# Performance work log

Measured on AMD Instinct MI355X. Metric: run time of the kernel, lower is better.

The kernel has to match this reference:

```python
import jax, jax.numpy as jnp
import numpy as np
from jax import lax

B, H, W = 1, 128, 128
KS = 3
N = KS * KS  # 9 deformable sampling points
BN_EPS = 1e-5


def conv2d(x, w, padding=0, stride=1):
    return lax.conv_general_dilated(x, w, (stride, stride),
                                    [(padding, padding), (padding, padding)],
                                    dimension_numbers=('NCHW', 'OIHW', 'NCHW'))


def bn_eval(x, gamma, beta, mean, var):
    scale = gamma / jnp.sqrt(var + BN_EPS)
    return x * scale[None, :, None, None] + (beta - mean * scale)[None, :, None, None]


def upsample_bilinear_ac(x, oh, ow):
    # F.interpolate(mode='bilinear', align_corners=True), separable gather
    b, c, h, w = x.shape
    ys = jnp.linspace(0.0, h - 1.0, oh)
    xs = jnp.linspace(0.0, w - 1.0, ow)
    y0 = jnp.floor(ys).astype(jnp.int32)
    y1 = jnp.minimum(y0 + 1, h - 1)
    wy = (ys - y0).astype(x.dtype)[None, None, :, None]
    x0 = jnp.floor(xs).astype(jnp.int32)
    x1 = jnp.minimum(x0 + 1, w - 1)
    wx = (xs - x0).astype(x.dtype)
    r = x[:, :, y0, :] * (1.0 - wy) + x[:, :, y1, :] * wy
    return r[:, :, :, x0] * (1.0 - wx) + r[:, :, :, x1] * wx


def deform_conv(x, p_w, p_b, dc_w, pad=1):
    # DeformConv2d(inc, outc, ks=3, padding=1, modulation=False):
    # offsets from a 3x3 conv, bilinear gather at p0 + p_n + offset on the
    # zero-padded input, then 3x3 kernel contraction over the 9 samples.
    b, c, h, w = x.shape
    off = conv2d(x, p_w, padding=1) + p_b[None, :, None, None]  # (b, 2N, h, w)
    rng = jnp.arange(KS, dtype=x.dtype) - (KS - 1) // 2          # [-1, 0, 1]
    pnx, pny = jnp.meshgrid(rng, rng, indexing='ij')
    # absolute sampling coords in padded frame, (b, h, w, N)
    px = jnp.transpose(off[:, :N], (0, 2, 3, 1)) + pnx.ravel() + jnp.arange(1, h + 1, dtype=x.dtype)[None, :, None, None]
    py = jnp.transpose(off[:, N:], (0, 2, 3, 1)) + pny.ravel() + jnp.arange(1, w + 1, dtype=x.dtype)[None, None, :, None]
    Hp, Wp = h + 2 * pad, w + 2 * pad
    xp = jnp.pad(x, ((0, 0), (0, 0), (pad, pad), (pad, pad))).reshape(b, c, Hp * Wp)
    fx = jnp.floor(px)
    fy = jnp.floor(py)
    x0f = jnp.clip(fx, 0, Hp - 1)
    x1f = jnp.clip(fx + 1.0, 0, Hp - 1)
    y0f = jnp.clip(fy, 0, Wp - 1)
    y1f = jnp.clip(fy + 1.0, 0, Wp - 1)
    pxc = jnp.clip(px, 0, Hp - 1)
    pyc = jnp.clip(py, 0, Wp - 1)

    def gather(qxf, qyf):
        idx = (qxf.astype(jnp.int32) * Wp + qyf.astype(jnp.int32)).reshape(b, 1, h * w * N)
        g = jnp.take_along_axis(xp, jnp.broadcast_to(idx, (b, c, h * w * N)), axis=2)
        return g.reshape(b, c, h, w, N)

    g_lt = (1.0 + (x0f - pxc)) * (1.0 + (y0f - pyc))
    g_rb = (1.0 - (x1f - pxc)) * (1.0 - (y1f - pyc))
    g_lb = (1.0 + (x0f - pxc)) * (1.0 - (y1f - pyc))
    g_rt = (1.0 - (x1f - pxc)) * (1.0 + (y0f - pyc))
    x_off = (g_lt[:, None] * gather(x0f, y0f) + g_rb[:, None] * gather(x1f, y1f)
             + g_lb[:, None] * gather(x0f, y1f) + g_rt[:, None] * gather(x1f, y0f))
    # conv(kernel=3, stride=3) on the rearranged samples == contraction over N
    return jnp.einsum('bchwk,ock->bohw', x_off, dc_w.reshape(dc_w.shape[0], c, N))


def _forward(x, low_level_feat, fm_w, fs_w, p_w, p_b, dc_w,
             lc1_w, bn1_gamma, bn1_beta, bn1_mean, bn1_var,
             lc2_w, bn2_gamma, bn2_beta, bn2_mean, bn2_var):
    xu = upsample_bilinear_ac(x, H, W)                       # (B,256,128,128)
    Z = low_level_feat                                       # AdaptiveAvgPool2d((128,128)) is identity on 128x128 input
    v = jax.nn.sigmoid(jnp.einsum('oc,bchw->bohw', fm_w, Z))
    u = jnp.einsum('bchk,bckw->bchw', low_level_feat, v) + low_level_feat
    Cf = jnp.einsum('oc,bchw->bohw', fs_w, u)
    cc = jnp.concatenate([xu, Cf], axis=1)                   # (B,512,128,128)
    fam = deform_conv(cc, p_w, p_b, dc_w) + Cf
    up1 = jax.nn.relu(bn_eval(conv2d(fam, lc1_w, padding=1), bn1_gamma, bn1_beta, bn1_mean, bn1_var))
    up2 = jax.nn.relu(bn_eval(conv2d(up1, lc2_w, padding=1), bn2_gamma, bn2_beta, bn2_mean, bn2_var))
    return up1, up2


def setup_inputs():
    key = jax.random.key(0)
    ks = jax.random.split(key, 12)
    f32 = jnp.float32
    return {
        'x': jax.random.normal(ks[0], (B, 256, 32, 32), f32),
        'low_level_feat': jax.random.normal(ks[1], (B, 256, H, W), f32),
        'fm_w': jax.random.normal(ks[2], (256, 256), f32) * 0.0625,
        'fs_w': jax.random.normal(ks[3], (256, 256), f32) * 0.0625,
        'p_w': jax.random.normal(ks[4], (2 * N, 512, 3, 3), f32) * 0.01,
        'p_b': jnp.zeros((2 * N,), f32),
        'dc_w': jax.random.normal(ks[5], (256, 512, 3, 3), f32) * 0.02,
        'lc1_w': jax.random.normal(ks[6], (256, 256, 3, 3), f32) * 0.02,
        'bn1_gamma': jnp.ones((256,), f32),
        'bn1_beta': jnp.zeros((256,), f32),
        'bn1_mean': jax.random.normal(ks[7], (256,), f32) * 0.1,
        'bn1_var': jax.random.uniform(ks[8], (256,), f32) + 0.5,
        'lc2_w': jax.random.normal(ks[9], (256, 256, 3, 3), f32) * 0.02,
        'bn2_gamma': jnp.ones((256,), f32),
        'bn2_beta': jnp.zeros((256,), f32),
        'bn2_mean': jax.random.normal(ks[10], (256,), f32) * 0.1,
        'bn2_var': jax.random.uniform(ks[11], (256,), f32) + 0.5,
    }


def reference(x, low_level_feat, fm_w, fs_w, p_w, p_b, dc_w,
              lc1_w, bn1_gamma, bn1_beta, bn1_mean, bn1_var,
              lc2_w, bn2_gamma, bn2_beta, bn2_mean, bn2_var):
    return _forward(x, low_level_feat, fm_w, fs_w, p_w, p_b, dc_w,
                    lc1_w, bn1_gamma, bn1_beta, bn1_mean, bn1_var,
                    lc2_w, bn2_gamma, bn2_beta, bn2_mean, bn2_var)
```

## Files before the change

### kernel.cpp

```cpp
#include <hip/hip_runtime.h>
#include <math.h>

#define HW   16384
#define PS   16900

typedef __attribute__((ext_vector_type(8))) short bf16x8;
typedef __attribute__((ext_vector_type(4))) float f32x4;

__device__ inline unsigned short f2bf(float x) {
    unsigned int u = __float_as_uint(x);
    unsigned int r = (u + 0x7fffu + ((u >> 16) & 1u)) >> 16;
    return (unsigned short)r;
}
__device__ inline float bf2f(unsigned short h) {
    return __uint_as_float(((unsigned int)h) << 16);
}

__global__ __launch_bounds__(256) void zero_ringP_k(unsigned short* __restrict__ base) {
    int t = blockIdx.x * 256 + threadIdx.x;
    if (t >= 520 * 32) return;
    int ck = (t & 31) << 3, rp = t >> 5;
    int row, col;
    if (rp < 130)      { row = 0;   col = rp; }
    else if (rp < 260) { row = 129; col = rp - 130; }
    else {
        int rem = rp - 260;
        if (rem >= 256) return;
        row = 1 + (rem >> 1); col = (rem & 1) ? 129 : 0;
    }
    bf16x8 z = (bf16x8){0, 0, 0, 0, 0, 0, 0, 0};
    *(bf16x8*)(base + (size_t)(row * 130 + col) * 256 + ck) = z;
}

__global__ __launch_bounds__(256) void ringT_k(unsigned short* __restrict__ ccT) {
    int t = blockIdx.x * 256 + threadIdx.x;
    if (t >= 520 * 256) return;
    int ci = t & 255, rp = t >> 8;
    int row, col;
    if (rp < 130)      { row = 0;   col = rp; }
    else if (rp < 260) { row = 129; col = rp - 130; }
    else {
        int rem = rp - 260;
        if (rem >= 256) return;
        row = 1 + (rem >> 1); col = (rem & 1) ? 129 : 0;
    }
    ccT[(size_t)(row * 130 + col) * 512 + 256 + ci] = 0;
}

__global__ __launch_bounds__(256) void upsample_k(const float* __restrict__ x,
                                                  float* __restrict__ ccpad) {
    int c = blockIdx.y;
    int idx = blockIdx.x * 256 + threadIdx.x;
    if (idx >= PS) return;
    int r = idx / 130, s = idx - r * 130;
    float val = 0.0f;
    if (r >= 1 && r <= 128 && s >= 1 && s <= 128) {
        int i = r - 1, j = s - 1;
        float yf = (float)i * (31.0f / 127.0f);
        float xf = (float)j * (31.0f / 127.0f);
        int y0 = min((int)yf, 31); int y1 = min(y0 + 1, 31);
        int x0 = min((int)xf, 31); int x1 = min(x0 + 1, 31);
        float wy = yf - (float)y0, wx = xf - (float)x0;
        const float* xc = x + (size_t)c * 1024;
        float a = xc[y0 * 32 + x0] * (1.0f - wx) + xc[y0 * 32 + x1] * wx;
        float b = xc[y1 * 32 + x0] * (1.0f - wx) + xc[y1 * 32 + x1] * wx;
        val = a * (1.0f - wy) + b * wy;
    }
    ccpad[(size_t)c * PS + idx] = val;
}

__global__ __launch_bounds__(256) void cvtT_flat_k(const float* __restrict__ src,
                                                   unsigned short* __restrict__ dst,
                                                   int npx) {
    int t = blockIdx.x * 256 + threadIdx.x;
    int c = t & 255, pix = t >> 8;
    dst[t] = f2bf(src[(size_t)c * npx + pix]);
}

__global__ __launch_bounds__(256) void cvtT_k(const float* __restrict__ src,
                                              unsigned short* __restrict__ dst) {
    int t = blockIdx.x * 256 + threadIdx.x;
    int c = t & 255, pix = t >> 8;
    dst[(size_t)pix * 512 + c] = f2bf(src[(size_t)c * PS + pix]);
}

__global__ __launch_bounds__(256) void w2bf_k(const float* __restrict__ a,
                                              const float* __restrict__ b,
                                              unsigned short* __restrict__ da,
                                              unsigned short* __restrict__ db) {
    int t = blockIdx.x * 256 + threadIdx.x;
    if (t >= 65536) return;
    da[t] = f2bf(a[t]);
    db[t] = f2bf(b[t]);
}

__global__ __launch_bounds__(256) void u_matmul_k(const float* __restrict__ llf,
                                                  const float* __restrict__ v,
                                                  float* __restrict__ u) {
    int c = blockIdx.y;
    const float* L = llf + (size_t)c * HW;
    const float* V = v   + (size_t)c * HW;
    float*       U = u   + (size_t)c * HW;
    int tid = threadIdx.x;
    int ty = tid >> 4, tx = tid & 15;
    int r0 = (blockIdx.x << 6) + (ty << 2);
    int w0 = tx << 3;
    float acc[4][8] = {};
    for (int k = 0; k < 128; ++k) {
        float a[4];
#pragma unroll
        for (int i = 0; i < 4; ++i) a[i] = L[(r0 + i) * 128 + k];
        float4 b0 = *(const float4*)(V + k * 128 + w0);
        float4 b1 = *(const float4*)(V + k * 128 + w0 + 4);
        float bv[8] = {b0.x, b0.y, b0.z, b0.w, b1.x, b1.y, b1.z, b1.w};
#pragma unroll
        for (int i = 0; i < 4; ++i)
#pragma unroll
            for (int j = 0; j < 8; ++j) acc[i][j] += a[i] * bv[j];
    }
#pragma unroll
    for (int i = 0; i < 4; ++i) {
#pragma unroll
        for (int j = 0; j < 8; ++j) acc[i][j] += L[(r0 + i) * 128 + w0 + j];
        *(float4*)(U + (r0 + i) * 128 + w0)     = make_float4(acc[i][0], acc[i][1], acc[i][2], acc[i][3]);
        *(float4*)(U + (r0 + i) * 128 + w0 + 4) = make_float4(acc[i][4], acc[i][5], acc[i][6], acc[i][7]);
    }
}

__global__ __launch_bounds__(256) void tr_ocK_k(const float* __restrict__ w,
                                                unsigned short* __restrict__ dst, int C) {
    int t = blockIdx.x * 256 + threadIdx.x;
    if (t >= 9 * 256 * C) return;
    int c = t % C; int rest = t / C; int o = rest & 255; int k = rest >> 8;
    dst[t] = f2bf(w[(size_t)o * C * 9 + c * 9 + k]);
}

__global__ __launch_bounds__(256) void tr_lcF_k(const float* __restrict__ w,
                                                unsigned short* __restrict__ dst) {
    int t = blockIdx.x * 256 + threadIdx.x;
    if (t >= 589824) return;
    int e    = t & 7;
    int lane = (t >> 3) & 63;
    int mi   = (t >> 9) & 3;
    int kss  = (t >> 11) & 7;
    int wo   = (t >> 14) & 3;
    int kt   = t >> 16;
    int o = (wo << 6) + (mi << 4) + (lane & 15);
    int c = (kss << 5) + ((lane >> 4) << 3) + e;
    dst[t] = f2bf(w[(size_t)o * 2304 + c * 9 + kt]);
}

__global__ __launch_bounds__(256) void tr_pw_k(const float* __restrict__ w,
                                               unsigned short* __restrict__ dst) {
    int t = blockIdx.x * 256 + threadIdx.x;
    if (t >= 9 * 32 * 512) return;
    int c = t & 511; int rest = t >> 9; int o = rest & 31; int k = rest >> 5;
    dst[t] = (o < 18) ? f2bf(w[(size_t)o * 4608 + c * 9 + k]) : (unsigned short)0;
}

__global__ __launch_bounds__(256, 2) void vmfma_k(
        const unsigned short* __restrict__ inT,
        const unsigned short* __restrict__ wh,
        float* __restrict__ vout) {
    __shared__ __align__(16) unsigned short Bs[32][72];
    int b = blockIdx.x;
    int xcd = b & 7, sl = b >> 3;
    int nt = (xcd << 6) + sl;
    int hrow = nt >> 2, pc0 = (nt & 3) << 5;
    int tid = threadIdx.x;
    int wv = tid >> 6, lane = tid & 63;
    int lr = lane & 15, lg = lane >> 4;
    int pxs = tid >> 3, cg8 = tid & 7;
    int p = (hrow << 7) + pc0 + pxs;
    f32x4 acc[4][2];
#pragma unroll
    for (int i = 0; i < 4; ++i)
#pragma unroll
        for (int j = 0; j < 2; ++j) acc[i][j] = (f32x4){0.f, 0.f, 0.f, 0.f};
    for (int ks = 0; ks < 256; ks += 64) {
        __syncthreads();
        *(bf16x8*)&Bs[pxs][cg8 << 3] =
            *(const bf16x8*)(inT + (size_t)p * 256 + ks + (cg8 << 3));
        __syncthreads();
#pragma unroll
        for (int s = 0; s < 2; ++s) {
            int ko = ks + (s << 5) + (lg << 3);
            bf16x8 af[4], bfr[2];
#pragma unroll
            for (int mi = 0; mi < 4; ++mi)
                af[mi] = *(const bf16x8*)(wh + (size_t)((wv << 6) + (mi << 4) + lr) * 256 + ko);
#pragma unroll
            for (int ni = 0; ni < 2; ++ni)
                bfr[ni] = *(const bf16x8*)(&Bs[(ni << 4) + lr][(s << 5) + (lg << 3)]);
#pragma unroll
            for (int mi = 0; mi < 4; ++mi)
#pragma unroll
                for (int ni = 0; ni < 2; ++ni)
                    acc[mi][ni] = __builtin_amdgcn_mfma_f32_16x16x32_bf16(
                        af[mi], bfr[ni], acc[mi][ni], 0, 0, 0);
        }
    }
#pragma unroll
    for (int mi = 0; mi < 4; ++mi)
#pragma unroll
        for (int ni = 0; ni < 2; ++ni)
#pragma unroll
            for (int r = 0; r < 4; ++r) {
                int o   = (wv << 6) + (mi << 4) + (lg << 2) + r;
                int pxx = pc0 + (ni << 4) + lr;
                vout[(size_t)o * HW + (hrow << 7) + pxx] =
                    1.0f / (1.0f + expf(-acc[mi][ni][r]));
            }
}

__global__ __launch_bounds__(256, 2) void cfmfma_k(
        const unsigned short* __restrict__ inT,
        const unsigned short* __restrict__ wh,
        unsigned short* __restrict__ ccT) {
    __shared__ __align__(16) unsigned short Bs[32][72];
    int b = blockIdx.x;
    int xcd = b & 7, sl = b >> 3;
    int nt = (xcd << 6) + sl;
    int hrow = nt >> 2, pc0 = (nt & 3) << 5;
    int tid = threadIdx.x;
    int wv = tid >> 6, lane = tid & 63;
    int lr = lane & 15, lg = lane >> 4;
    int pxs = tid >> 3, cg8 = tid & 7;
    int p = (hrow << 7) + pc0 + pxs;
    f32x4 acc[4][2];
#pragma unroll
    for (int i = 0; i < 4; ++i)
#pragma unroll
        for (int j = 0; j < 2; ++j) acc[i][j] = (f32x4){0.f, 0.f, 0.f, 0.f};
    for (int ks = 0; ks < 256; ks += 64) {
        __syncthreads();
        *(bf16x8*)&Bs[pxs][cg8 << 3] =
            *(const bf16x8*)(inT + (size_t)p * 256 + ks + (cg8 << 3));
        __syncthreads();
#pragma unroll
        for (int s = 0; s < 2; ++s) {
            int ko = ks + (s << 5) + (lg << 3);
            bf16x8 af[4], bfr[2];
#pragma unroll
            for (int mi = 0; mi < 4; ++mi)
                af[mi] = *(const bf16x8*)(wh + (size_t)((wv << 6) + (mi << 4) + lr) * 256 + ko);
#pragma unroll
            for (int ni = 0; ni < 2; ++ni)
                bfr[ni] = *(const bf16x8*)(&Bs[(ni << 4) + lr][(s << 5) + (lg << 3)]);
#pragma unroll
            for (int mi = 0; mi < 4; ++mi)
#pragma unroll
                for (int ni = 0; ni < 2; ++ni)
                    acc[mi][ni] = __builtin_amdgcn_mfma_f32_16x16x32_bf16(
                        af[mi], bfr[ni], acc[mi][ni], 0, 0, 0);
        }
    }
#pragma unroll
    for (int mi = 0; mi < 4; ++mi)
#pragma unroll
        for (int ni = 0; ni < 2; ++ni) {
            int pxx = pc0 + (ni << 4) + lr;
            int pix = (hrow + 1) * 130 + pxx + 1;
            unsigned short pk[4];
#pragma unroll
            for (int r = 0; r < 4; ++r) pk[r] = f2bf(acc[mi][ni][r]);
            *(ushort4*)(ccT + (size_t)pix * 512 + 256 + (wv << 6) + (mi << 4) + (lg << 2))
                = *(ushort4*)pk;
        }
}

__global__ __launch_bounds__(256, 2) void off_part_k(
        const unsigned short* __restrict__ ccT,
        const unsigned short* __restrict__ pwTh,
        float* __restrict__ pbuf) {
    __shared__ __align__(16) unsigned short Bs[128][40];
    int b = blockIdx.x;
    int xcd = b & 7, slot = b >> 3;
    int hrow = (xcd << 4) + (slot >> 2);
    int cg = slot & 3, c0 = cg << 7;
    int tid = threadIdx.x;
    int wv = tid >> 6, lane = tid & 63;
    int wr = wv >> 1, wc = wv & 1;
    int lr = lane & 15, lg = lane >> 4;
    int c4 = tid & 3, pxs = tid >> 2;
    f32x4 acc[4];
#pragma unroll
    for (int j = 0; j < 4; ++j) acc[j] = (f32x4){0.f, 0.f, 0.f, 0.f};

    for (int kt = 0; kt < 9; ++kt) {
        int dy = kt / 3 - 1, dx = kt % 3 - 1;
        int pixb = (hrow + dy + 1) * 130 + dx + 1;
        for (int ksl = 0; ksl < 128; ksl += 32) {
            __syncthreads();
#pragma unroll
            for (int pp = 0; pp < 2; ++pp) {
                int px = pxs + (pp << 6);
                *(bf16x8*)&Bs[px][c4 << 3] =
                    *(const bf16x8*)(ccT + (size_t)(pixb + px) * 512 + c0 + ksl + (c4 << 3));
            }
            __syncthreads();
            bf16x8 af, bfr[4];
            af = *(const bf16x8*)(pwTh + (size_t)kt * 16384
                                  + (size_t)((wr << 4) + lr) * 512 + c0 + ksl + (lg << 3));
#pragma unroll
            for (int ni = 0; ni < 4; ++ni) {
                int n = (wc << 6) + (ni << 4) + lr;
                bfr[ni] = *(const bf16x8*)(&Bs[n][lg << 3]);
            }
#pragma unroll
            for (int ni = 0; ni < 4; ++ni)
                acc[ni] = __builtin_amdgcn_mfma_f32_16x16x32_bf16(af, bfr[ni], acc[ni], 0, 0, 0);
        }
    }
#pragma unroll
    for (int ni = 0; ni < 4; ++ni)
#pragma unroll
        for (int r = 0; r < 4; ++r) {
            int o = (wr << 4) + (lg << 2) + r;
            int p = (hrow << 7) + (wc << 6) + (ni << 4) + lr;
            pbuf[(size_t)((cg << 5) + o) * HW + p] = acc[ni][r];
        }
}

__global__ __launch_bounds__(256) void make_idx_k(const float* __restrict__ pbuf,
                                                  const float* __restrict__ pb,
                                                  int4* __restrict__ IDX,
                                                  float4* __restrict__ WT) {
    int t = blockIdx.x * 256 + threadIdx.x;
    if (t >= 9 * HW) return;
    int k = t >> 14, p = t & 16383;
    int h = p >> 7, w = p & 127;
    float ox = 0.f, oy = 0.f;
#pragma unroll
    for (int cg = 0; cg < 4; ++cg) {
        ox += pbuf[(size_t)((cg << 5) + k) * HW + p];
        oy += pbuf[(size_t)((cg << 5) + 9 + k) * HW + p];
    }
    float px = ox + pb[k]     + (float)(k / 3 - 1) + (float)(h + 1);
    float py = oy + pb[9 + k] + (float)(k % 3 - 1) + (float)(w + 1);
    float fx = floorf(px), fy = floorf(py);
    float x0 = fminf(fmaxf(fx,        0.f), 129.f);
    float x1 = fminf(fmaxf(fx + 1.0f, 0.f), 129.f);
    float y0 = fminf(fmaxf(fy,        0.f), 129.f);
    float y1 = fminf(fmaxf(fy + 1.0f, 0.f), 129.f);
    float pxc = fminf(fmaxf(px, 0.f), 129.f);
    float pyc = fminf(fmaxf(py, 0.f), 129.f);
    float gx0 = 1.0f + x0 - pxc, gx1 = 1.0f - x1 + pxc;
    float gy0 = 1.0f + y0 - pyc, gy1 = 1.0f - y1 + pyc;
    int ix0 = (int)x0, ix1 = (int)x1, iy0 = (int)y0, iy1 = (int)y1;
    IDX[t] = make_int4((ix0 * 130 + iy0) << 9, (ix1 * 130 + iy1) << 9,
                       (ix0 * 130 + iy1) << 9, (ix1 * 130 + iy0) << 9);
    WT[t]  = make_float4(gx0 * gy0, gx1 * gy1, gx0 * gy1, gx1 * gy0);
}

__global__ __launch_bounds__(512, 4) void fam8_k(
        const unsigned short* __restrict__ ccT,
        const unsigned short* __restrict__ dcwTh,
        const int4* __restrict__ IDX, const float4* __restrict__ WT,
        unsigned short* __restrict__ part0,
        unsigned short* __restrict__ part1) {
    __shared__ __align__(16) unsigned short As[256][72];
    __shared__ __align__(16) unsigned short Bs[64][72];
    int b = blockIdx.x;
    int khalf = b >> 8;
    int bb = b & 255;
    int xcd = bb & 7, sl = bb >> 3;
    int nt = (xcd << 5) + sl;
    int hrow = nt >> 1, pc0 = (nt & 1) << 6;
    int tid = threadIdx.x;
    int wv = tid >> 6, lane = tid & 63;
    int wo = wv >> 1, wp = wv & 1;
    int lr = lane & 15, lg = lane >> 4;
    int pxg = tid >> 3, grp = tid & 7;
    int p2 = (hrow << 7) + pc0 + pxg;
    f32x4 acc[4][2];
#pragma unroll
    for (int i = 0; i < 4; ++i)
#pragma unroll
        for (int j = 0; j < 2; ++j) acc[i][j] = (f32x4){0.f, 0.f, 0.f, 0.f};

    bf16x8 a0, a1, a2, a3, v0, v1, v2, v3;

#define ISSUE_A(ch) do {                                                      \
    const unsigned short* dwk_ = dcwTh + (size_t)((ch) >> 3) * 131072         \
                                       + (((ch) & 7) << 6);                   \
    a0 = *(const bf16x8*)(dwk_ + (size_t)(pxg      ) * 512 + (grp << 3));     \
    a1 = *(const bf16x8*)(dwk_ + (size_t)(pxg +  64) * 512 + (grp << 3));     \
    a2 = *(const bf16x8*)(dwk_ + (size_t)(pxg + 128) * 512 + (grp << 3));     \
    a3 = *(const bf16x8*)(dwk_ + (size_t)(pxg + 192) * 512 + (grp << 3));     \
} while (0)

#define ISSUE_G(ch, idm) do {                                                 \
    int cb_ = (((ch) & 7) << 6) + (grp << 3);                                 \
    v0 = *(const bf16x8*)(ccT + (idm).x + cb_);                               \
    v1 = *(const bf16x8*)(ccT + (idm).y + cb_);                               \
    v2 = *(const bf16x8*)(ccT + (idm).z + cb_);                               \
    v3 = *(const bf16x8*)(ccT + (idm).w + cb_);                               \
} while (0)

    int c0 = khalf * 36, c1 = c0 + 36;
    int kt0 = c0 >> 3;
    int4   idc = IDX[(kt0 << 14) + p2];
    float4 wtc = WT [(kt0 << 14) + p2];
    int4   idn = IDX[((kt0 + 1) << 14) + p2];
    float4 wtn = WT [((kt0 + 1) << 14) + p2];
    ISSUE_A(c0);
    ISSUE_G(c0, idc);
    float4 wcur = wtc;

    for (int c = c0; c < c1; ++c) {
        __syncthreads();
        *(bf16x8*)&As[pxg      ][grp << 3] = a0;
        *(bf16x8*)&As[pxg +  64][grp << 3] = a1;
        *(bf16x8*)&As[pxg + 128][grp << 3] = a2;
        *(bf16x8*)&As[pxg + 192][grp << 3] = a3;
        {
            unsigned short pk[8];
#pragma unroll
            for (int e = 0; e < 8; ++e) {
                float val = wcur.x * bf2f((unsigned short)v0[e])
                          + wcur.y * bf2f((unsigned short)v1[e])
                          + wcur.z * bf2f((unsigned short)v2[e])
                          + wcur.w * bf2f((unsigned short)v3[e]);
                pk[e] = f2bf(val);
            }
            *(bf16x8*)&Bs[pxg][grp << 3] = *(bf16x8*)pk;
        }
        int cn = c + 1;
        if (cn < c1) {
            if ((cn & 7) == 0) {
                idc = idn; wtc = wtn;
                int kt2 = (cn >> 3) + 1;
                if ((kt2 << 3) < c1) {
                    idn = IDX[(kt2 << 14) + p2];
                    wtn = WT [(kt2 << 14) + p2];
                }
            }
            ISSUE_A(cn);
            ISSUE_G(cn, idc);
            wcur = wtc;
        }
        __syncthreads();
#pragma unroll
        for (int s = 0; s < 2; ++s) {
            int ko = (s << 5) + (lg << 3);
            bf16x8 af[4], bfr[2];
#pragma unroll
            for (int mi = 0; mi < 4; ++mi)
                af[mi] = *(const bf16x8*)(&As[(wo << 6) + (mi << 4) + lr][ko]);
#pragma unroll
            for (int ni = 0; ni < 2; ++ni)
                bfr[ni] = *(const bf16x8*)(&Bs[(wp << 5) + (ni << 4) + lr][ko]);
#pragma unroll
            for (int mi = 0; mi < 4; ++mi)
#pragma unroll
                for (int ni = 0; ni < 2; ++ni)
                    acc[mi][ni] = __builtin_amdgcn_mfma_f32_16x16x32_bf16(
                        af[mi], bfr[ni], acc[mi][ni], 0, 0, 0);
        }
    }
#undef ISSUE_A
#undef ISSUE_G

    unsigned short* pt = khalf ? part1 : part0;
#pragma unroll
    for (int mi = 0; mi < 4; ++mi)
#pragma unroll
        for (int ni = 0; ni < 2; ++ni) {
            int pxx = pc0 + (wp << 5) + (ni << 4) + lr;
            int p = (hrow << 7) + pxx;
            unsigned short pk[4];
#pragma unroll
            for (int r = 0; r < 4; ++r) pk[r] = f2bf(acc[mi][ni][r]);
            *(ushort4*)(pt + (size_t)p * 256 + (wo << 6) + (mi << 4) + (lg << 2))
                = *(ushort4*)pk;
        }
}

__global__ __launch_bounds__(256) void combineT_k(
        const unsigned short* __restrict__ p0,
        const unsigned short* __restrict__ p1,
        const unsigned short* __restrict__ ccT,
        unsigned short* __restrict__ famT) {
    int t = blockIdx.x * 256 + threadIdx.x;
    int o8 = (t & 31) << 3, p = t >> 5;
    int row = p >> 7, col = p & 127;
    int pix = (row + 1) * 130 + col + 1;
    bf16x8 a = *(const bf16x8*)(p0 + (size_t)p * 256 + o8);
    bf16x8 b = *(const bf16x8*)(p1 + (size_t)p * 256 + o8);
    bf16x8 c = *(const bf16x8*)(ccT + (size_t)pix * 512 + 256 + o8);
    unsigned short out[8];
#pragma unroll
    for (int e = 0; e < 8; ++e)
        out[e] = f2bf(bf2f((unsigned short)a[e]) + bf2f((unsigned short)b[e])
                      + bf2f((unsigned short)c[e]));
    *(bf16x8*)(famT + (size_t)pix * 256 + o8) = *(bf16x8*)out;
}

__global__ __launch_bounds__(256, 2) void conv2T_k(
        const unsigned short* __restrict__ inT,
        const unsigned short* __restrict__ wF,
        const float* __restrict__ gam, const float* __restrict__ bet,
        const float* __restrict__ mean, const float* __restrict__ var,
        float* __restrict__ out_flat,
        unsigned short* __restrict__ out_padT) {
    __shared__ __align__(16) unsigned short Ls[102][264];
    __shared__ float scs[256], bis[256];
    int b = blockIdx.x;
    int xcd = b & 7, slot = b >> 3;
    int nt = (xcd << 6) + slot;
    int hrow = nt >> 2, pc0 = (nt & 3) << 5;
    int tid = threadIdx.x;
    int wv = tid >> 6, lane = tid & 63;
    int lr = lane & 15, lg = lane >> 4;
    {
        float sc = gam[tid] * rsqrtf(var[tid] + 1e-5f);
        scs[tid] = sc;
        bis[tid] = bet[tid] - mean[tid] * sc;
    }
#pragma unroll
    for (int r = 0; r < 3; ++r) {
        const unsigned short* src = inT + (size_t)((hrow + r) * 130 + pc0) * 256;
#pragma unroll
        for (int ps = 0; ps < 5; ++ps) {
            int idx = ps * 2048 + tid * 8;
            if (idx < 8704) {
                bf16x8 v = *(const bf16x8*)(src + idx);
                *(bf16x8*)&Ls[r * 34 + (idx >> 8)][idx & 255] = v;
            }
        }
    }
    __syncthreads();

    f32x4 acc[4][2];
#pragma unroll
    for (int i = 0; i < 4; ++i)
#pragma unroll
        for (int j = 0; j < 2; ++j) acc[i][j] = (f32x4){0.f, 0.f, 0.f, 0.f};

    const unsigned short* wvb = wF + ((size_t)wv << 14) + ((size_t)lane << 3);
    for (int kt = 0; kt < 9; ++kt) {
        int rowb = (kt / 3) * 34 + (kt % 3);
        const unsigned short* wkb = wvb + (size_t)kt * 65536;
#pragma unroll
        for (int kss = 0; kss < 8; ++kss) {
            int ks = kss << 5;
            bf16x8 af[4], bfr[2];
#pragma unroll
            for (int mi = 0; mi < 4; ++mi)
                af[mi] = *(const bf16x8*)(wkb + (size_t)kss * 2048 + mi * 512);
#pragma unroll
            for (int ni = 0; ni < 2; ++ni)
                bfr[ni] = *(const bf16x8*)(&Ls[rowb + (ni << 4) + lr][ks + (lg << 3)]);
#pragma unroll
            for (int mi = 0; mi < 4; ++mi)
#pragma unroll
                for (int ni = 0; ni < 2; ++ni)
                    acc[mi][ni] = __builtin_amdgcn_mfma_f32_16x16x32_bf16(
                        af[mi], bfr[ni], acc[mi][ni], 0, 0, 0);
        }
    }

#pragma unroll
    for (int mi = 0; mi < 4; ++mi)
#pragma unroll
        for (int ni = 0; ni < 2; ++ni) {
            int pxx = pc0 + (ni << 4) + lr;
            unsigned short pk[4];
#pragma unroll
            for (int r = 0; r < 4; ++r) {
                int o = (wv << 6) + (mi << 4) + (lg << 2) + r;
                float rv = fmaxf(acc[mi][ni][r] * scs[o] + bis[o], 0.0f);
                out_flat[(size_t)o * HW + (hrow << 7) + pxx] = rv;
                pk[r] = f2bf(rv);
            }
            if (out_padT) {
                int pix = (hrow + 1) * 130 + pxx + 1;
                *(ushort4*)(out_padT + (size_t)pix * 256 + (wv << 6) + (mi << 4) + (lg << 2))
                    = *(ushort4*)pk;
            }
        }
}

extern "C" void kernel_launch(void* const* d_in, const int* in_sizes, int n_in,
                              void* d_out, int out_size, void* d_ws, size_t ws_size,
                              hipStream_t stream) {
    const float* x     = (const float*)d_in[0];
    const float* llf   = (const float*)d_in[1];
    const float* fm_w  = (const float*)d_in[2];
    const float* fs_w  = (const float*)d_in[3];
    const float* p_w   = (const float*)d_in[4];
    const float* p_b   = (const float*)d_in[5];
    const float* dc_w  = (const float*)d_in[6];
    const float* lc1_w = (const float*)d_in[7];
    const float* bn1g  = (const float*)d_in[8];
    const float* bn1b  = (const float*)d_in[9];
    const float* bn1m  = (const float*)d_in[10];
    const float* bn1v  = (const float*)d_in[11];
    const float* lc2_w = (const float*)d_in[12];
    const float* bn2g  = (const float*)d_in[13];
    const float* bn2b  = (const float*)d_in[14];
    const float* bn2m  = (const float*)d_in[15];
    const float* bn2v  = (const float*)d_in[16];
    float* out1 = (float*)d_out;
    float* out2 = out1 + (size_t)256 * HW;

    if (ws_size < 79839232u) return;
    char* ws = (char*)d_ws;
    unsigned short* ccT   = (unsigned short*)ws;
    float*          ccpad = (float*)(ws + 17305600);
    float*          vbuf  = (float*)(ws + 17305600);
    unsigned short* famT  = (unsigned short*)(ws + 17305600);
    unsigned short* up1T  = (unsigned short*)(ws + 26091520);
    unsigned short* llfT  = (unsigned short*)(ws + 34877440);
    unsigned short* uT    = (unsigned short*)(ws + 43266048);
    unsigned short* part0 = (unsigned short*)(ws + 43266048);
    unsigned short* fmwh  = (unsigned short*)(ws + 51654656);
    unsigned short* fswh  = (unsigned short*)(ws + 51785728);
    float*          ubuf  = (float*)(ws + 51916800);
    float*          pbuf  = (float*)(ws + 51916800);
    unsigned short* part1 = (unsigned short*)(ws + 51916800);
    int4*           IDX   = (int4*)  (ws + 60305408);
    float4*         WT    = (float4*)(ws + 62664704);
    unsigned short* dcwTh  = (unsigned short*)(ws + 68694016);
    unsigned short* lcw1F  = (unsigned short*)(ws + 71053312);
    unsigned short* lcw2F  = (unsigned short*)(ws + 72232960);
    unsigned short* pwTh   = (unsigned short*)(ws + 73412608);

    upsample_k<<<dim3(67, 256), 256, 0, stream>>>(x, ccpad);
    cvtT_k<<<dim3(16900), 256, 0, stream>>>(ccpad, ccT);
    cvtT_flat_k<<<dim3(16384), 256, 0, stream>>>(llf, llfT, HW);
    w2bf_k<<<dim3(256), 256, 0, stream>>>(fm_w, fs_w, fmwh, fswh);
    vmfma_k<<<dim3(512), 256, 0, stream>>>(llfT, fmwh, vbuf);
    u_matmul_k<<<dim3(2, 256), 256, 0, stream>>>(llf, vbuf, ubuf);
    cvtT_flat_k<<<dim3(16384), 256, 0, stream>>>(ubuf, uT, HW);
    tr_ocK_k<<<dim3(4608), 256, 0, stream>>>(dc_w, dcwTh, 512);
    tr_lcF_k<<<dim3(2304), 256, 0, stream>>>(lc1_w, lcw1F);
    tr_lcF_k<<<dim3(2304), 256, 0, stream>>>(lc2_w, lcw2F);
    tr_pw_k<<<dim3(576), 256, 0, stream>>>(p_w, pwTh);
    cfmfma_k<<<dim3(512), 256, 0, stream>>>(uT, fswh, ccT);
    ringT_k<<<dim3(520), 256, 0, stream>>>(ccT);
    off_part_k<<<dim3(512), 256, 0, stream>>>(ccT, pwTh, pbuf);
    make_idx_k<<<dim3(576), 256, 0, stream>>>(pbuf, p_b, IDX, WT);
    zero_ringP_k<<<dim3(65), 256, 0, stream>>>(famT);
    zero_ringP_k<<<dim3(65), 256, 0, stream>>>(up1T);
    fam8_k<<<dim3(512), 512, 0, stream>>>(ccT, dcwTh, IDX, WT, part0, part1);
    combineT_k<<<dim3(2048), 256, 0, stream>>>(part0, part1, ccT, famT);
    conv2T_k<<<dim3(512), 256, 0, stream>>>(famT, lcw1F, bn1g, bn1b, bn1m, bn1v,
                                            out1, up1T);
    conv2T_k<<<dim3(512), 256, 0, stream>>>(up1T, lcw2F, bn2g, bn2b, bn2m, bn2v,
                                            out2, nullptr);
}
```

Before: 459.8 us.

## Load deform-conv weights directly into MFMA fragments and double-buffer the sample tile

The deformable conv weights are pre-swizzled into a per-wave MFMA fragment layout, so each wave loads its A operands straight from global memory into registers instead of staging a 256x64 tile through shared memory. The sampled-input tile is double-buffered in LDS so that publishing chunk c+1 overlaps the MFMAs of chunk c. Each wave now owns 32 output channels across all 64 pixels rather than 64x32. This removes LDS traffic and one write phase for the weights, at the cost of more global loads per wave and higher register pressure.

```diff
diff --git a/kernel.cpp b/kernel.cpp
--- a/kernel.cpp
+++ b/kernel.cpp
@@ -127,12 +127,21 @@
     }
 }
 
-__global__ __launch_bounds__(256) void tr_ocK_k(const float* __restrict__ w,
-                                                unsigned short* __restrict__ dst, int C) {
-    int t = blockIdx.x * 256 + threadIdx.x;
-    if (t >= 9 * 256 * C) return;
-    int c = t % C; int rest = t / C; int o = rest & 255; int k = rest >> 8;
-    dst[t] = f2bf(w[(size_t)o * C * 9 + c * 9 + k]);
+__global__ __launch_bounds__(256) void tr_dcwF9_k(const float* __restrict__ w,
+                                                  unsigned short* __restrict__ dst) {
+    int t = blockIdx.x * 256 + threadIdx.x;
+    if (t >= 1179648) return;
+    int e    = t & 7;
+    int lane = (t >> 3) & 63;
+    int f    = t >> 9;
+    int mi   = f & 1;
+    int s    = (f >> 1) & 1;
+    int wv   = (f >> 2) & 7;
+    int ch   = f >> 5;
+    int kt   = ch >> 3;
+    int o = (wv << 5) + (mi << 4) + (lane & 15);
+    int c = ((ch & 7) << 6) + (s << 5) + ((lane >> 4) << 3) + e;
+    dst[t] = f2bf(w[(size_t)o * 4608 + c * 9 + kt]);
 }
 
 __global__ __launch_bounds__(256) void tr_lcF_k(const float* __restrict__ w,
@@ -353,14 +362,13 @@
     WT[t]  = make_float4(gx0 * gy0, gx1 * gy1, gx0 * gy1, gx1 * gy0);
 }
 
-__global__ __launch_bounds__(512, 4) void fam8_k(
+__global__ __launch_bounds__(512, 4) void fam9_k(
         const unsigned short* __restrict__ ccT,
-        const unsigned short* __restrict__ dcwTh,
+        const unsigned short* __restrict__ dcwF,
         const int4* __restrict__ IDX, const float4* __restrict__ WT,
         unsigned short* __restrict__ part0,
         unsigned short* __restrict__ part1) {
-    __shared__ __align__(16) unsigned short As[256][72];
-    __shared__ __align__(16) unsigned short Bs[64][72];
+    __shared__ __align__(16) unsigned short Bs[2][64][72];
     int b = blockIdx.x;
     int khalf = b >> 8;
     int bb = b & 255;
@@ -369,28 +377,29 @@
     int hrow = nt >> 1, pc0 = (nt & 1) << 6;
     int tid = threadIdx.x;
     int wv = tid >> 6, lane = tid & 63;
-    int wo = wv >> 1, wp = wv & 1;
     int lr = lane & 15, lg = lane >> 4;
     int pxg = tid >> 3, grp = tid & 7;
     int p2 = (hrow << 7) + pc0 + pxg;
-    f32x4 acc[4][2];
-#pragma unroll
-    for (int i = 0; i < 4; ++i)
-#pragma unroll
-        for (int j = 0; j < 2; ++j) acc[i][j] = (f32x4){0.f, 0.f, 0.f, 0.f};
-
-    bf16x8 a0, a1, a2, a3, v0, v1, v2, v3;
-
-#define ISSUE_A(ch) do {                                                      \
-    const unsigned short* dwk_ = dcwTh + (size_t)((ch) >> 3) * 131072         \
-                                       + (((ch) & 7) << 6);                   \
-    a0 = *(const bf16x8*)(dwk_ + (size_t)(pxg      ) * 512 + (grp << 3));     \
-    a1 = *(const bf16x8*)(dwk_ + (size_t)(pxg +  64) * 512 + (grp << 3));     \
-    a2 = *(const bf16x8*)(dwk_ + (size_t)(pxg + 128) * 512 + (grp << 3));     \
-    a3 = *(const bf16x8*)(dwk_ + (size_t)(pxg + 192) * 512 + (grp << 3));     \
+    const unsigned short* wfb = dcwF + ((size_t)wv << 11) + ((size_t)lane << 3);
+    f32x4 acc[2][4];
+#pragma unroll
+    for (int i = 0; i < 2; ++i)
+#pragma unroll
+        for (int j = 0; j < 4; ++j) acc[i][j] = (f32x4){0.f, 0.f, 0.f, 0.f};
+
+    bf16x8 v0, v1, v2, v3;
+    bf16x8 Aa00, Aa01, Aa10, Aa11;
+    bf16x8 Ba00, Ba01, Ba10, Ba11;
+
+#define ISSUE_A9(S, ch) do {                                                  \
+    const unsigned short* ap_ = wfb + ((size_t)(ch) << 14);                   \
+    S##00 = *(const bf16x8*)(ap_);                                            \
+    S##01 = *(const bf16x8*)(ap_ + 512);                                      \
+    S##10 = *(const bf16x8*)(ap_ + 1024);                                     \
+    S##11 = *(const bf16x8*)(ap_ + 1536);                                     \
 } while (0)
 
-#define ISSUE_G(ch, idm) do {                                                 \
+#define ISSUE_G9(ch, idm) do {                                                \
     int cb_ = (((ch) & 7) << 6) + (grp << 3);                                 \
     v0 = *(const bf16x8*)(ccT + (idm).x + cb_);                               \
     v1 = *(const bf16x8*)(ccT + (idm).y + cb_);                               \
@@ -398,81 +407,90 @@
     v3 = *(const bf16x8*)(ccT + (idm).w + cb_);                               \
 } while (0)
 
+#define NEXT_G9(cn) do {                                                      \
+    if ((cn) < c1) {                                                          \
+        if (((cn) & 7) == 0) {                                                \
+            idc = idn; wtc = wtn;                                             \
+            int kt2_ = ((cn) >> 3) + 1;                                       \
+            if ((kt2_ << 3) < c1) {                                           \
+                idn = IDX[(kt2_ << 14) + p2];                                 \
+                wtn = WT [(kt2_ << 14) + p2];                                 \
+            }                                                                 \
+        }                                                                     \
+        ISSUE_G9(cn, idc);                                                    \
+        wnext = wtc;                                                          \
+    }                                                                         \
+} while (0)
+
+#define PUBLISH9(bi) do {                                                     \
+    unsigned short pk_[8];                                                    \
+    _Pragma("unroll")                                                         \
+    for (int e_ = 0; e_ < 8; ++e_) {                                          \
+        float val_ = wcur.x * bf2f((unsigned short)v0[e_])                    \
+                   + wcur.y * bf2f((unsigned short)v1[e_])                    \
+                   + wcur.z * bf2f((unsigned short)v2[e_])                    \
+                   + wcur.w * bf2f((unsigned short)v3[e_]);                   \
+        pk_[e_] = f2bf(val_);                                                 \
+    }                                                                         \
+    *(bf16x8*)&Bs[bi][pxg][grp << 3] = *(bf16x8*)pk_;                         \
+} while (0)
+
+#define MFMA9(S, bi) do {                                                     \
+    _Pragma("unroll")                                                         \
+    for (int ni_ = 0; ni_ < 4; ++ni_) {                                       \
+        bf16x8 b0_ = *(const bf16x8*)(&Bs[bi][(ni_ << 4) + lr][lg << 3]);     \
+        acc[0][ni_] = __builtin_amdgcn_mfma_f32_16x16x32_bf16(S##00, b0_, acc[0][ni_], 0, 0, 0); \
+        acc[1][ni_] = __builtin_amdgcn_mfma_f32_16x16x32_bf16(S##01, b0_, acc[1][ni_], 0, 0, 0); \
+    }                                                                         \
+    _Pragma("unroll")                                                         \
+    for (int ni_ = 0; ni_ < 4; ++ni_) {                                       \
+        bf16x8 b1_ = *(const bf16x8*)(&Bs[bi][(ni_ << 4) + lr][32 + (lg << 3)]); \
+        acc[0][ni_] = __builtin_amdgcn_mfma_f32_16x16x32_bf16(S##10, b1_, acc[0][ni_], 0, 0, 0); \
+        acc[1][ni_] = __builtin_amdgcn_mfma_f32_16x16x32_bf16(S##11, b1_, acc[1][ni_], 0, 0, 0); \
+    }                                                                         \
+} while (0)
+
     int c0 = khalf * 36, c1 = c0 + 36;
     int kt0 = c0 >> 3;
     int4   idc = IDX[(kt0 << 14) + p2];
     float4 wtc = WT [(kt0 << 14) + p2];
     int4   idn = IDX[((kt0 + 1) << 14) + p2];
     float4 wtn = WT [((kt0 + 1) << 14) + p2];
-    ISSUE_A(c0);
-    ISSUE_G(c0, idc);
-    float4 wcur = wtc;
-
-    for (int c = c0; c < c1; ++c) {
+    ISSUE_G9(c0, idc);
+    float4 wcur = wtc, wnext = wtc;
+    ISSUE_A9(Aa, c0);
+
+    for (int c = c0; c < c1; c += 2) {
+        PUBLISH9(0);
+        NEXT_G9(c + 1);
+        ISSUE_A9(Ba, c + 1);
         __syncthreads();
-        *(bf16x8*)&As[pxg      ][grp << 3] = a0;
-        *(bf16x8*)&As[pxg +  64][grp << 3] = a1;
-        *(bf16x8*)&As[pxg + 128][grp << 3] = a2;
-        *(bf16x8*)&As[pxg + 192][grp << 3] = a3;
-        {
-            unsigned short pk[8];
-#pragma unroll
-            for (int e = 0; e < 8; ++e) {
-                float val = wcur.x * bf2f((unsigned short)v0[e])
-                          + wcur.y * bf2f((unsigned short)v1[e])
-                          + wcur.z * bf2f((unsigned short)v2[e])
-                          + wcur.w * bf2f((unsigned short)v3[e]);
-                pk[e] = f2bf(val);
-            }
-            *(bf16x8*)&Bs[pxg][grp << 3] = *(bf16x8*)pk;
-        }
-        int cn = c + 1;
-        if (cn < c1) {
-            if ((cn & 7) == 0) {
-                idc = idn; wtc = wtn;
-                int kt2 = (cn >> 3) + 1;
-                if ((kt2 << 3) < c1) {
-                    idn = IDX[(kt2 << 14) + p2];
-                    wtn = WT [(kt2 << 14) + p2];
-                }
-            }
-            ISSUE_A(cn);
-            ISSUE_G(cn, idc);
-            wcur = wtc;
-        }
+        MFMA9(Aa, 0);
+        wcur = wnext;
+        PUBLISH9(1);
+        NEXT_G9(c + 2);
+        if (c + 2 < c1) ISSUE_A9(Aa, c + 2);
         __syncthreads();
-#pragma unroll
-        for (int s = 0; s < 2; ++s) {
-            int ko = (s << 5) + (lg << 3);
-            bf16x8 af[4], bfr[2];
-#pragma unroll
-            for (int mi = 0; mi < 4; ++mi)
-                af[mi] = *(const bf16x8*)(&As[(wo << 6) + (mi << 4) + lr][ko]);
-#pragma unroll
-            for (int ni = 0; ni < 2; ++ni)
-                bfr[ni] = *(const bf16x8*)(&Bs[(wp << 5) + (ni << 4) + lr][ko]);
-#pragma unroll
-            for (int mi = 0; mi < 4; ++mi)
-#pragma unroll
-                for (int ni = 0; ni < 2; ++ni)
-                    acc[mi][ni] = __builtin_amdgcn_mfma_f32_16x16x32_bf16(
-                        af[mi], bfr[ni], acc[mi][ni], 0, 0, 0);
-        }
-    }
-#undef ISSUE_A
-#undef ISSUE_G
+        MFMA9(Ba, 1);
+        wcur = wnext;
+    }
+#undef ISSUE_A9
+#undef ISSUE_G9
+#undef NEXT_G9
+#undef PUBLISH9
+#undef MFMA9
 
     unsigned short* pt = khalf ? part1 : part0;
 #pragma unroll
-    for (int mi = 0; mi < 4; ++mi)
-#pragma unroll
-        for (int ni = 0; ni < 2; ++ni) {
-            int pxx = pc0 + (wp << 5) + (ni << 4) + lr;
+    for (int mi = 0; mi < 2; ++mi)
+#pragma unroll
+        for (int ni = 0; ni < 4; ++ni) {
+            int pxx = pc0 + (ni << 4) + lr;
             int p = (hrow << 7) + pxx;
             unsigned short pk[4];
 #pragma unroll
             for (int r = 0; r < 4; ++r) pk[r] = f2bf(acc[mi][ni][r]);
-            *(ushort4*)(pt + (size_t)p * 256 + (wo << 6) + (mi << 4) + (lg << 2))
+            *(ushort4*)(pt + (size_t)p * 256 + (wv << 5) + (mi << 4) + (lg << 2))
                 = *(ushort4*)pk;
         }
 }
@@ -622,7 +640,7 @@
     unsigned short* part1 = (unsigned short*)(ws + 51916800);
     int4*           IDX   = (int4*)  (ws + 60305408);
     float4*         WT    = (float4*)(ws + 62664704);
-    unsigned short* dcwTh  = (unsigned short*)(ws + 68694016);
+    unsigned short* dcwF   = (unsigned short*)(ws + 68694016);
     unsigned short* lcw1F  = (unsigned short*)(ws + 71053312);
     unsigned short* lcw2F  = (unsigned short*)(ws + 72232960);
     unsigned short* pwTh   = (unsigned short*)(ws + 73412608);
@@ -634,7 +652,7 @@
     vmfma_k<<<dim3(512), 256, 0, stream>>>(llfT, fmwh, vbuf);
     u_matmul_k<<<dim3(2, 256), 256, 0, stream>>>(llf, vbuf, ubuf);
     cvtT_flat_k<<<dim3(16384), 256, 0, stream>>>(ubuf, uT, HW);
-    tr_ocK_k<<<dim3(4608), 256, 0, stream>>>(dc_w, dcwTh, 512);
+    tr_dcwF9_k<<<dim3(4608), 256, 0, stream>>>(dc_w, dcwF);
     tr_lcF_k<<<dim3(2304), 256, 0, stream>>>(lc1_w, lcw1F);
     tr_lcF_k<<<dim3(2304), 256, 0, stream>>>(lc2_w, lcw2F);
     tr_pw_k<<<dim3(576), 256, 0, stream>>>(p_w, pwTh);
@@ -644,7 +662,7 @@
     make_idx_k<<<dim3(576), 256, 0, stream>>>(pbuf, p_b, IDX, WT);
     zero_ringP_k<<<dim3(65), 256, 0, stream>>>(famT);
     zero_ringP_k<<<dim3(65), 256, 0, stream>>>(up1T);
-    fam8_k<<<dim3(512), 512, 0, stream>>>(ccT, dcwTh, IDX, WT, part0, part1);
+    fam9_k<<<dim3(512), 512, 0, stream>>>(ccT, dcwF, IDX, WT, part0, part1);
     combineT_k<<<dim3(2048), 256, 0, stream>>>(part0, part1, ccT, famT);
     conv2T_k<<<dim3(512), 256, 0, stream>>>(famT, lcw1F, bn1g, bn1b, bn1m, bn1v,
                                             out1, up1T);
```

New measurement: 451.0 us. About the same (-1.9%).
